# Kernel optimization log

Hardware: AMD Instinct MI355X
Metric: run time of the kernel (lower is better)

The kernel has to match this reference:

```python
import jax, jax.numpy as jnp
import numpy as np

N_NODES = 100000
N_EDGES = 600000
F_IN, HID, CLS = 128, 128, 16


def sage_conv(x, src, dst, W_l, b_l, W_r, n_nodes):
    # mean aggregation of neighbor features: message x[src] scattered to dst
    msg = x[src]                                              # [E, F]
    agg = jax.ops.segment_sum(msg, dst, num_segments=n_nodes)  # [N, F]
    deg = jax.ops.segment_sum(jnp.ones((src.shape[0],), x.dtype), dst, num_segments=n_nodes)
    agg = agg / jnp.maximum(deg, 1.0)[:, None]
    # PyG SAGEConv: lin_l(agg) (with bias) + lin_r(x_root) (no bias)
    return agg @ W_l + b_l + x @ W_r


def setup_inputs() -> dict:
    key = jax.random.key(0)
    ks = jax.random.split(key, 6)
    x = jax.random.normal(ks[0], (N_NODES, F_IN), jnp.float32)
    edge_index = jax.random.randint(ks[1], (2, N_EDGES), 0, N_NODES, dtype=jnp.int64)
    s1 = 1.0 / np.sqrt(F_IN)
    s2 = 1.0 / np.sqrt(HID)
    return {
        "x": x,
        "edge_index": edge_index,
        "W1_l": jax.random.normal(ks[2], (F_IN, HID), jnp.float32) * s1,
        "b1": jnp.zeros((HID,), jnp.float32),
        "W1_r": jax.random.normal(ks[3], (F_IN, HID), jnp.float32) * s1,
        "W2_l": jax.random.normal(ks[4], (HID, CLS), jnp.float32) * s2,
        "b2": jnp.zeros((CLS,), jnp.float32),
        "W2_r": jax.random.normal(ks[5], (HID, CLS), jnp.float32) * s2,
    }


def reference(x, edge_index, W1_l, b1, W1_r, W2_l, b2, W2_r):
    n = x.shape[0]
    src, dst = edge_index[0], edge_index[1]
    h = sage_conv(x, src, dst, W1_l, b1, W1_r, n)
    h = jax.nn.relu(h)
    # F.dropout(training=self.training): identity in eval mode
    out = sage_conv(h, src, dst, W2_l, b2, W2_r, n)
    return jax.nn.log_softmax(out, axis=1)
```

## Files before the change

kernel.cpp:

```cpp
#include <hip/hip_runtime.h>
#include <cstdint>

#define N_NODES 100000
#define N_PAD 100096
#define N_EDGES 600000
#define F 128
#define CLS 16
#define CAP 32

typedef short bf16x8 __attribute__((ext_vector_type(8)));
typedef float f32x4 __attribute__((ext_vector_type(4)));

__device__ inline float bf2f(unsigned int lo16) { return __uint_as_float(lo16 << 16); }
__device__ inline unsigned short f2b(float f) {
    unsigned int u = __float_as_uint(f);
    return (unsigned short)((u + 0x7fffu + ((u >> 16) & 1u)) >> 16);
}

__global__ __launch_bounds__(256) void prep_k(const int* __restrict__ src,
                                              const int* __restrict__ dst,
                                              int* __restrict__ deg,
                                              int* __restrict__ bucket,
                                              const float* __restrict__ x,
                                              unsigned short* __restrict__ xb,
                                              const float* __restrict__ W1l,
                                              const float* __restrict__ W1r,
                                              const float* __restrict__ W2l,
                                              const float* __restrict__ W2r,
                                              unsigned short* __restrict__ w1t,
                                              unsigned short* __restrict__ w2t) {
    int b = blockIdx.x;
    if (b < 2344) {
        int e = b * 256 + threadIdx.x;
        if (e < N_EDGES) {
            int d = dst[e];
            int slot = atomicAdd(&deg[d], 1);
            if (slot < CAP) bucket[d * CAP + slot] = src[e];
        }
    } else if (b < 14844) {
        int i = (b - 2344) * 256 + threadIdx.x;
        float4 v = ((const float4*)x)[i];
        ushort4 o;
        o.x = f2b(v.x); o.y = f2b(v.y); o.z = f2b(v.z); o.w = f2b(v.w);
        ((ushort4*)xb)[i] = o;
    } else if (b < 14972) {
        int idx = (b - 14844) * 256 + threadIdx.x;
        int n = idx >> 8, k = idx & 255;
        float v = (k < F) ? W1l[k * F + n] : W1r[(k - F) * F + n];
        int ct = n >> 4, m = n & 15;
        int half = k >> 7, ks = (k >> 5) & 3, quad = (k >> 3) & 3, j = k & 7;
        w1t[(ct * 8 + ks * 2 + half) * 512 + (quad * 16 + m) * 8 + j] = f2b(v);
    } else {
        int idx = (b - 14972) * 256 + threadIdx.x;
        if (idx < 32 * F) {
            int n = idx >> 7, k = idx & 127;
            float v = (n < CLS) ? W2l[k * CLS + n] : W2r[k * CLS + (n - CLS)];
            int tile = n >> 4, m = n & 15;
            int ks = (k >> 5) & 3, quad = (k >> 3) & 3, j = k & 7;
            w2t[(tile * 4 + ks) * 512 + (quad * 16 + m) * 8 + j] = f2b(v);
        }
    }
}

__global__ __launch_bounds__(256) void gemm_fused(const unsigned short* __restrict__ Xb,
                                                  const int* __restrict__ deg,
                                                  const int* __restrict__ bucket,
                                                  const unsigned short* __restrict__ Wt,
                                                  const float* __restrict__ bias,
                                                  const unsigned short* __restrict__ Wt2,
                                                  unsigned short* __restrict__ trLb,
                                                  float* __restrict__ trR) {
    __shared__ unsigned short sh[128 * 136];
    int tid = threadIdx.x;
    int row0 = blockIdx.x * 128;

    {
        int ns = tid >> 1, half = tid & 1;
        const int4* gsrc = (const int4*)(bucket + (size_t)(row0 + ns) * CAP + half * 16);
        int* drow = (int*)(sh + ns * 136);
        int4* ldst = (int4*)(drow + half * 16);
        ldst[0] = gsrc[0];
        ldst[1] = gsrc[1];
        ldst[2] = gsrc[2];
        ldst[3] = gsrc[3];
        if (half == 0) drow[32] = deg[row0 + ns];
    }

    int grp = tid >> 5, c4 = (tid & 31) * 4;
    int lrb = grp * 16;

#define ISSUE(P, DV, LR) do { \
    const int* brow_ = (const int*)(sh + (LR) * 136); \
    int node_ = row0 + (LR); \
    int draw_ = brow_[32]; \
    DV = (node_ < N_NODES) ? min(max(draw_, 0), CAP) : 0; \
    int4 b0_ = ((const int4*)brow_)[0]; \
    int4 b1_ = ((const int4*)brow_)[1]; \
    int4 b2_ = ((const int4*)brow_)[2]; \
    int n0_  = (DV > 0 ) ? min(max(b0_.x, 0), N_NODES - 1) : 0; \
    int n1_  = (DV > 1 ) ? min(max(b0_.y, 0), N_NODES - 1) : 0; \
    int n2_  = (DV > 2 ) ? min(max(b0_.z, 0), N_NODES - 1) : 0; \
    int n3_  = (DV > 3 ) ? min(max(b0_.w, 0), N_NODES - 1) : 0; \
    int n4_  = (DV > 4 ) ? min(max(b1_.x, 0), N_NODES - 1) : 0; \
    int n5_  = (DV > 5 ) ? min(max(b1_.y, 0), N_NODES - 1) : 0; \
    int n6_  = (DV > 6 ) ? min(max(b1_.z, 0), N_NODES - 1) : 0; \
    int n7_  = (DV > 7 ) ? min(max(b1_.w, 0), N_NODES - 1) : 0; \
    int n8_  = (DV > 8 ) ? min(max(b2_.x, 0), N_NODES - 1) : 0; \
    int n9_  = (DV > 9 ) ? min(max(b2_.y, 0), N_NODES - 1) : 0; \
    int n10_ = (DV > 10) ? min(max(b2_.z, 0), N_NODES - 1) : 0; \
    int n11_ = (DV > 11) ? min(max(b2_.w, 0), N_NODES - 1) : 0; \
    P##0  = *(const uint2*)(Xb + (size_t)n0_  * F + c4); \
    P##1  = *(const uint2*)(Xb + (size_t)n1_  * F + c4); \
    P##2  = *(const uint2*)(Xb + (size_t)n2_  * F + c4); \
    P##3  = *(const uint2*)(Xb + (size_t)n3_  * F + c4); \
    P##4  = *(const uint2*)(Xb + (size_t)n4_  * F + c4); \
    P##5  = *(const uint2*)(Xb + (size_t)n5_  * F + c4); \
    P##6  = *(const uint2*)(Xb + (size_t)n6_  * F + c4); \
    P##7  = *(const uint2*)(Xb + (size_t)n7_  * F + c4); \
    P##8  = *(const uint2*)(Xb + (size_t)n8_  * F + c4); \
    P##9  = *(const uint2*)(Xb + (size_t)n9_  * F + c4); \
    P##10 = *(const uint2*)(Xb + (size_t)n10_ * F + c4); \
    P##11 = *(const uint2*)(Xb + (size_t)n11_ * F + c4); \
} while (0)

#define ACC4(vv) { \
    acc_[0] += bf2f((vv).x & 0xffffu); acc_[1] += bf2f((vv).x >> 16); \
    acc_[2] += bf2f((vv).y & 0xffffu); acc_[3] += bf2f((vv).y >> 16); }

#define CONSUME(P, DV, LR) do { \
    float acc_[4] = {0.f, 0.f, 0.f, 0.f}; \
    if (DV > 0)  ACC4(P##0); \
    if (DV > 1)  ACC4(P##1); \
    if (DV > 2)  ACC4(P##2); \
    if (DV > 3)  ACC4(P##3); \
    if (DV > 4)  ACC4(P##4); \
    if (DV > 5)  ACC4(P##5); \
    if (DV > 6)  ACC4(P##6); \
    if (DV > 7)  ACC4(P##7); \
    if (DV > 8)  ACC4(P##8); \
    if (DV > 9)  ACC4(P##9); \
    if (DV > 10) ACC4(P##10); \
    if (DV > 11) ACC4(P##11); \
    if (DV > 12) { \
        const int* brow_ = (const int*)(sh + (LR) * 136); \
        for (int j0 = 12; j0 < DV; j0 += 4) { \
            int4 bb_ = *(const int4*)(brow_ + j0); \
            int rem_ = DV - j0; \
            int m0_ = (rem_ > 0) ? min(max(bb_.x, 0), N_NODES - 1) : 0; \
            int m1_ = (rem_ > 1) ? min(max(bb_.y, 0), N_NODES - 1) : 0; \
            int m2_ = (rem_ > 2) ? min(max(bb_.z, 0), N_NODES - 1) : 0; \
            int m3_ = (rem_ > 3) ? min(max(bb_.w, 0), N_NODES - 1) : 0; \
            uint2 w0_ = *(const uint2*)(Xb + (size_t)m0_ * F + c4); \
            uint2 w1_ = *(const uint2*)(Xb + (size_t)m1_ * F + c4); \
            uint2 w2_ = *(const uint2*)(Xb + (size_t)m2_ * F + c4); \
            uint2 w3_ = *(const uint2*)(Xb + (size_t)m3_ * F + c4); \
            if (rem_ > 0) ACC4(w0_); \
            if (rem_ > 1) ACC4(w1_); \
            if (rem_ > 2) ACC4(w2_); \
            if (rem_ > 3) ACC4(w3_); \
        } \
    } \
    float inv_ = 1.0f / fmaxf((float)DV, 1.0f); \
    uint2 o_; \
    o_.x = (unsigned int)f2b(acc_[0] * inv_) | ((unsigned int)f2b(acc_[1] * inv_) << 16); \
    o_.y = (unsigned int)f2b(acc_[2] * inv_) | ((unsigned int)f2b(acc_[3] * inv_) << 16); \
    *(uint2*)&sh[(LR) * 136 + c4] = o_; \
} while (0)

    {
        uint2 vA0, vA1, vA2, vA3, vA4, vA5, vA6, vA7, vA8, vA9, vA10, vA11;
        uint2 vB0, vB1, vB2, vB3, vB4, vB5, vB6, vB7, vB8, vB9, vB10, vB11;
        int dA, dB;
        ISSUE(vA, dA, lrb + 0);
        ISSUE(vB, dB, lrb + 1);
#pragma unroll 1
        for (int rr = 0; rr < 14; rr += 2) {
            CONSUME(vA, dA, lrb + rr);
            ISSUE(vA, dA, lrb + rr + 2);
            CONSUME(vB, dB, lrb + rr + 1);
            ISSUE(vB, dB, lrb + rr + 3);
        }
        CONSUME(vA, dA, lrb + 14);
        CONSUME(vB, dB, lrb + 15);
    }
#undef ISSUE
#undef ACC4
#undef CONSUME
    __syncthreads();

    int wave = tid >> 6, lane = tid & 63;
    int m = lane & 15, quad = lane >> 4;
    int koff = quad * 8;
    int wrow0 = row0 + wave * 32;

    const unsigned short* sa0 = sh + (wave * 32 + m) * 136 + koff;
    const unsigned short* sa1 = sa0 + 16 * 136;
    const unsigned short* px0 = Xb + (size_t)(wrow0 + m) * F + koff;
    const unsigned short* px1 = px0 + 16 * F;
    const unsigned short* pw = Wt + lane * 8;

    f32x4 acc0[8], acc1[8];
#pragma unroll
    for (int ct = 0; ct < 8; ct++) { acc0[ct] = (f32x4){0,0,0,0}; acc1[ct] = (f32x4){0,0,0,0}; }

#pragma unroll
    for (int ks = 0; ks < 4; ks++) {
        bf16x8 a0 = *(const bf16x8*)(const void*)(sa0 + ks * 32);
        bf16x8 a1 = *(const bf16x8*)(const void*)(sa1 + ks * 32);
        bf16x8 x0 = *(const bf16x8*)(const void*)(px0 + ks * 32);
        bf16x8 x1 = *(const bf16x8*)(const void*)(px1 + ks * 32);
#pragma unroll
        for (int ct = 0; ct < 8; ct++) {
            bf16x8 bl = *(const bf16x8*)(const void*)(pw + (ct * 8 + ks * 2 + 0) * 512);
            bf16x8 br = *(const bf16x8*)(const void*)(pw + (ct * 8 + ks * 2 + 1) * 512);
            acc0[ct] = __builtin_amdgcn_mfma_f32_16x16x32_bf16(a0, bl, acc0[ct], 0, 0, 0);
            acc1[ct] = __builtin_amdgcn_mfma_f32_16x16x32_bf16(a1, bl, acc1[ct], 0, 0, 0);
            acc0[ct] = __builtin_amdgcn_mfma_f32_16x16x32_bf16(x0, br, acc0[ct], 0, 0, 0);
            acc1[ct] = __builtin_amdgcn_mfma_f32_16x16x32_bf16(x1, br, acc1[ct], 0, 0, 0);
        }
    }
    __syncthreads();

    int lr0 = wave * 32 + quad * 4;
#pragma unroll
    for (int ct = 0; ct < 8; ct++) {
        int n = ct * 16 + m;
        float bv = bias[n];
#pragma unroll
        for (int r = 0; r < 4; r++) {
            sh[(lr0 + r) * 136 + n]      = f2b(fmaxf(acc0[ct][r] + bv, 0.f));
            sh[(lr0 + 16 + r) * 136 + n] = f2b(fmaxf(acc1[ct][r] + bv, 0.f));
        }
    }
    __syncthreads();

    const unsigned short* hl0 = sh + (wave * 32 + m) * 136 + koff;
    const unsigned short* hl1 = hl0 + 16 * 136;
    const unsigned short* pw2 = Wt2 + lane * 8;

    f32x4 al0 = (f32x4){0,0,0,0}, al1 = (f32x4){0,0,0,0};
    f32x4 ar0 = (f32x4){0,0,0,0}, ar1 = (f32x4){0,0,0,0};
#pragma unroll
    for (int ks = 0; ks < 4; ks++) {
        bf16x8 h0 = *(const bf16x8*)(const void*)(hl0 + ks * 32);
        bf16x8 h1 = *(const bf16x8*)(const void*)(hl1 + ks * 32);
        bf16x8 wl = *(const bf16x8*)(const void*)(pw2 + (0 * 4 + ks) * 512);
        bf16x8 wr = *(const bf16x8*)(const void*)(pw2 + (1 * 4 + ks) * 512);
        al0 = __builtin_amdgcn_mfma_f32_16x16x32_bf16(h0, wl, al0, 0, 0, 0);
        al1 = __builtin_amdgcn_mfma_f32_16x16x32_bf16(h1, wl, al1, 0, 0, 0);
        ar0 = __builtin_amdgcn_mfma_f32_16x16x32_bf16(h0, wr, ar0, 0, 0, 0);
        ar1 = __builtin_amdgcn_mfma_f32_16x16x32_bf16(h1, wr, ar1, 0, 0, 0);
    }
    int r0 = wrow0 + quad * 4;
#pragma unroll
    for (int r = 0; r < 4; r++) {
        trLb[(size_t)(r0 + r) * CLS + m]      = f2b(al0[r]);
        trLb[(size_t)(r0 + 16 + r) * CLS + m] = f2b(al1[r]);
        trR[(size_t)(r0 + r) * CLS + m]       = ar0[r];
        trR[(size_t)(r0 + 16 + r) * CLS + m]  = ar1[r];
    }
}

__global__ __launch_bounds__(256) void agg2sm_k(const unsigned short* __restrict__ trLb,
                                                const float* __restrict__ trR,
                                                const int* __restrict__ deg,
                                                const int* __restrict__ bucket,
                                                const float* __restrict__ b2,
                                                float* __restrict__ out) {
    int node = blockIdx.x * 4 + (threadIdx.x >> 6);
    int lane = threadIdx.x & 63;
    int r = lane >> 2;
    int cq = (lane & 3) * 4;
    const int* bk = bucket + node * CAP;

    int d_raw = deg[node];
    int d = min(d_raw, CAP);
    int nb = (r < d) ? min(max(bk[r], 0), N_NODES - 1) : 0;
    uint2 v = *(const uint2*)(trLb + (size_t)nb * CLS + cq);
    float4 selfR = *(const float4*)(trR + (size_t)node * CLS + cq);

    float4 acc = {0.f, 0.f, 0.f, 0.f};
    if (r < d) {
        acc.x += bf2f(v.x & 0xffffu); acc.y += bf2f(v.x >> 16);
        acc.z += bf2f(v.y & 0xffffu); acc.w += bf2f(v.y >> 16);
    }
    if (d > 16) {
        int idx = 16 + r;
        bool valid = idx < d;
        int m2 = valid ? min(max(bk[idx], 0), N_NODES - 1) : 0;
        uint2 w = *(const uint2*)(trLb + (size_t)m2 * CLS + cq);
        if (valid) {
            acc.x += bf2f(w.x & 0xffffu); acc.y += bf2f(w.x >> 16);
            acc.z += bf2f(w.y & 0xffffu); acc.w += bf2f(w.y >> 16);
        }
    }
#pragma unroll
    for (int off = 4; off <= 32; off <<= 1) {
        acc.x += __shfl_xor(acc.x, off);
        acc.y += __shfl_xor(acc.y, off);
        acc.z += __shfl_xor(acc.z, off);
        acc.w += __shfl_xor(acc.w, off);
    }
    float inv = 1.0f / fmaxf((float)d, 1.0f);
    float4 bb = *(const float4*)(b2 + cq);
    float vx = acc.x * inv + selfR.x + bb.x;
    float vy = acc.y * inv + selfR.y + bb.y;
    float vz = acc.z * inv + selfR.z + bb.z;
    float vw = acc.w * inv + selfR.w + bb.w;
    float mx = fmaxf(fmaxf(vx, vy), fmaxf(vz, vw));
    mx = fmaxf(mx, __shfl_xor(mx, 1));
    mx = fmaxf(mx, __shfl_xor(mx, 2));
    float sm = __expf(vx - mx) + __expf(vy - mx) + __expf(vz - mx) + __expf(vw - mx);
    sm += __shfl_xor(sm, 1);
    sm += __shfl_xor(sm, 2);
    float lg = __logf(sm);
    if (r == 0) {
        float4 o = {vx - mx - lg, vy - mx - lg, vz - mx - lg, vw - mx - lg};
        *(float4*)(out + (size_t)node * CLS + cq) = o;
    }
}


extern "C" void kernel_launch(void* const* d_in, const int* in_sizes, int n_in,
                              void* d_out, int out_size, void* d_ws, size_t ws_size,
                              hipStream_t stream) {
    const float* x   = (const float*)d_in[0];
    const int*   ei  = (const int*)d_in[1];
    const float* W1l = (const float*)d_in[2];
    const float* b1  = (const float*)d_in[3];
    const float* W1r = (const float*)d_in[4];
    const float* W2l = (const float*)d_in[5];
    const float* b2  = (const float*)d_in[6];
    const float* W2r = (const float*)d_in[7];
    float* out = (float*)d_out;

    const int* src = ei;
    const int* dst = ei + N_EDGES;

    char* ws = (char*)d_ws;
    size_t off = 0;
    auto alloc = [&](size_t bytes) { char* p = ws + off; off += (bytes + 127) / 128 * 128; return p; };
    int* deg    = (int*)alloc((size_t)N_NODES * 4);
    int* bucket = (int*)alloc((size_t)N_NODES * CAP * 4);
    unsigned short* xb   = (unsigned short*)alloc((size_t)N_PAD * F * 2);
    unsigned short* trLb = (unsigned short*)alloc((size_t)N_PAD * CLS * 2);
    float*          trR  = (float*)alloc((size_t)N_PAD * CLS * 4);
    unsigned short* w1t  = (unsigned short*)alloc((size_t)F * 256 * 2);
    unsigned short* w2t  = (unsigned short*)alloc((size_t)32 * F * 2);

    hipMemsetAsync(deg, 0, (size_t)N_NODES * 4, stream);
    prep_k<<<14988, 256, 0, stream>>>(src, dst, deg, bucket, x, xb,
                                      W1l, W1r, W2l, W2r, w1t, w2t);
    gemm_fused<<<N_PAD / 128, 256, 0, stream>>>(xb, deg, bucket, w1t, b1, w2t, trLb, trR);
    agg2sm_k<<<N_NODES / 4, 256, 0, stream>>>(trLb, trR, deg, bucket, b2, out);
}
```

Measured before the change: 218.6 us.

## Gather neighbor rows into LDS via global_load_lds instead of register prefetch

Replaces the register-based software-pipelined neighbor gather (two nodes in flight, 12 uint2 loads each) with direct global-to-LDS 16-byte loads into a per-wave scratch buffer, then sums from LDS. Each wave handles two nodes per step, waiting on vmcnt(0) before consuming, so there is no overlap between gather and accumulate across steps. It aims to issue wider loads and reduce register pressure, at the cost of extra LDS usage (which may lower occupancy) and a serialized load-wait per step.

```diff
diff --git a/kernel.cpp b/kernel.cpp
--- a/kernel.cpp
+++ b/kernel.cpp
@@ -7,6 +7,7 @@
 #define F 128
 #define CLS 16
 #define CAP 32
+#define SLOTS 12
 
 typedef short bf16x8 __attribute__((ext_vector_type(8)));
 typedef float f32x4 __attribute__((ext_vector_type(4)));
@@ -71,8 +72,10 @@
                                                   unsigned short* __restrict__ trLb,
                                                   float* __restrict__ trR) {
     __shared__ unsigned short sh[128 * 136];
+    __shared__ unsigned short scr[4][2 * SLOTS * 128];
     int tid = threadIdx.x;
     int row0 = blockIdx.x * 128;
+    int wave = tid >> 6, lane = tid & 63;
 
     {
         int ns = tid >> 1, half = tid & 1;
@@ -86,109 +89,66 @@
         if (half == 0) drow[32] = deg[row0 + ns];
     }
 
-    int grp = tid >> 5, c4 = (tid & 31) * 4;
-    int lrb = grp * 16;
-
-#define ISSUE(P, DV, LR) do { \
-    const int* brow_ = (const int*)(sh + (LR) * 136); \
-    int node_ = row0 + (LR); \
-    int draw_ = brow_[32]; \
-    DV = (node_ < N_NODES) ? min(max(draw_, 0), CAP) : 0; \
-    int4 b0_ = ((const int4*)brow_)[0]; \
-    int4 b1_ = ((const int4*)brow_)[1]; \
-    int4 b2_ = ((const int4*)brow_)[2]; \
-    int n0_  = (DV > 0 ) ? min(max(b0_.x, 0), N_NODES - 1) : 0; \
-    int n1_  = (DV > 1 ) ? min(max(b0_.y, 0), N_NODES - 1) : 0; \
-    int n2_  = (DV > 2 ) ? min(max(b0_.z, 0), N_NODES - 1) : 0; \
-    int n3_  = (DV > 3 ) ? min(max(b0_.w, 0), N_NODES - 1) : 0; \
-    int n4_  = (DV > 4 ) ? min(max(b1_.x, 0), N_NODES - 1) : 0; \
-    int n5_  = (DV > 5 ) ? min(max(b1_.y, 0), N_NODES - 1) : 0; \
-    int n6_  = (DV > 6 ) ? min(max(b1_.z, 0), N_NODES - 1) : 0; \
-    int n7_  = (DV > 7 ) ? min(max(b1_.w, 0), N_NODES - 1) : 0; \
-    int n8_  = (DV > 8 ) ? min(max(b2_.x, 0), N_NODES - 1) : 0; \
-    int n9_  = (DV > 9 ) ? min(max(b2_.y, 0), N_NODES - 1) : 0; \
-    int n10_ = (DV > 10) ? min(max(b2_.z, 0), N_NODES - 1) : 0; \
-    int n11_ = (DV > 11) ? min(max(b2_.w, 0), N_NODES - 1) : 0; \
-    P##0  = *(const uint2*)(Xb + (size_t)n0_  * F + c4); \
-    P##1  = *(const uint2*)(Xb + (size_t)n1_  * F + c4); \
-    P##2  = *(const uint2*)(Xb + (size_t)n2_  * F + c4); \
-    P##3  = *(const uint2*)(Xb + (size_t)n3_  * F + c4); \
-    P##4  = *(const uint2*)(Xb + (size_t)n4_  * F + c4); \
-    P##5  = *(const uint2*)(Xb + (size_t)n5_  * F + c4); \
-    P##6  = *(const uint2*)(Xb + (size_t)n6_  * F + c4); \
-    P##7  = *(const uint2*)(Xb + (size_t)n7_  * F + c4); \
-    P##8  = *(const uint2*)(Xb + (size_t)n8_  * F + c4); \
-    P##9  = *(const uint2*)(Xb + (size_t)n9_  * F + c4); \
-    P##10 = *(const uint2*)(Xb + (size_t)n10_ * F + c4); \
-    P##11 = *(const uint2*)(Xb + (size_t)n11_ * F + c4); \
-} while (0)
-
-#define ACC4(vv) { \
-    acc_[0] += bf2f((vv).x & 0xffffu); acc_[1] += bf2f((vv).x >> 16); \
-    acc_[2] += bf2f((vv).y & 0xffffu); acc_[3] += bf2f((vv).y >> 16); }
-
-#define CONSUME(P, DV, LR) do { \
-    float acc_[4] = {0.f, 0.f, 0.f, 0.f}; \
-    if (DV > 0)  ACC4(P##0); \
-    if (DV > 1)  ACC4(P##1); \
-    if (DV > 2)  ACC4(P##2); \
-    if (DV > 3)  ACC4(P##3); \
-    if (DV > 4)  ACC4(P##4); \
-    if (DV > 5)  ACC4(P##5); \
-    if (DV > 6)  ACC4(P##6); \
-    if (DV > 7)  ACC4(P##7); \
-    if (DV > 8)  ACC4(P##8); \
-    if (DV > 9)  ACC4(P##9); \
-    if (DV > 10) ACC4(P##10); \
-    if (DV > 11) ACC4(P##11); \
-    if (DV > 12) { \
-        const int* brow_ = (const int*)(sh + (LR) * 136); \
-        for (int j0 = 12; j0 < DV; j0 += 4) { \
-            int4 bb_ = *(const int4*)(brow_ + j0); \
-            int rem_ = DV - j0; \
-            int m0_ = (rem_ > 0) ? min(max(bb_.x, 0), N_NODES - 1) : 0; \
-            int m1_ = (rem_ > 1) ? min(max(bb_.y, 0), N_NODES - 1) : 0; \
-            int m2_ = (rem_ > 2) ? min(max(bb_.z, 0), N_NODES - 1) : 0; \
-            int m3_ = (rem_ > 3) ? min(max(bb_.w, 0), N_NODES - 1) : 0; \
-            uint2 w0_ = *(const uint2*)(Xb + (size_t)m0_ * F + c4); \
-            uint2 w1_ = *(const uint2*)(Xb + (size_t)m1_ * F + c4); \
-            uint2 w2_ = *(const uint2*)(Xb + (size_t)m2_ * F + c4); \
-            uint2 w3_ = *(const uint2*)(Xb + (size_t)m3_ * F + c4); \
-            if (rem_ > 0) ACC4(w0_); \
-            if (rem_ > 1) ACC4(w1_); \
-            if (rem_ > 2) ACC4(w2_); \
-            if (rem_ > 3) ACC4(w3_); \
-        } \
-    } \
-    float inv_ = 1.0f / fmaxf((float)DV, 1.0f); \
-    uint2 o_; \
-    o_.x = (unsigned int)f2b(acc_[0] * inv_) | ((unsigned int)f2b(acc_[1] * inv_) << 16); \
-    o_.y = (unsigned int)f2b(acc_[2] * inv_) | ((unsigned int)f2b(acc_[3] * inv_) << 16); \
-    *(uint2*)&sh[(LR) * 136 + c4] = o_; \
-} while (0)
-
     {
-        uint2 vA0, vA1, vA2, vA3, vA4, vA5, vA6, vA7, vA8, vA9, vA10, vA11;
-        uint2 vB0, vB1, vB2, vB3, vB4, vB5, vB6, vB7, vB8, vB9, vB10, vB11;
-        int dA, dB;
-        ISSUE(vA, dA, lrb + 0);
-        ISSUE(vB, dB, lrb + 1);
+        int l4 = lane >> 4;
+        int c16 = (lane & 15) * 8;
+        int nis = lane >> 5;
+        int c4 = (lane & 31) * 4;
+        unsigned short* myscr = &scr[wave][0];
+
 #pragma unroll 1
-        for (int rr = 0; rr < 14; rr += 2) {
-            CONSUME(vA, dA, lrb + rr);
-            ISSUE(vA, dA, lrb + rr + 2);
-            CONSUME(vB, dB, lrb + rr + 1);
-            ISSUE(vB, dB, lrb + rr + 3);
-        }
-        CONSUME(vA, dA, lrb + 14);
-        CONSUME(vB, dB, lrb + 15);
-    }
-#undef ISSUE
-#undef ACC4
-#undef CONSUME
+        for (int sc = 0; sc < 16; ++sc) {
+            int lrA = wave * 32 + sc * 2;
+            int lrB = lrA + 1;
+            const int* browA = (const int*)(sh + lrA * 136);
+            const int* browB = (const int*)(sh + lrB * 136);
+            int dAr = browA[32], dBr = browB[32];
+            int dA = (row0 + lrA < N_NODES) ? min(max(dAr, 0), CAP) : 0;
+            int dB = (row0 + lrB < N_NODES) ? min(max(dBr, 0), CAP) : 0;
+
+#pragma unroll
+            for (int i = 0; i < 6; ++i) {
+                const int* brow = (i < 3) ? browA : browB;
+                int dcl = (i < 3) ? dA : dB;
+                int slot = (i < 3 ? i * 4 : (i - 3) * 4) + l4;
+                int bs = brow[slot];
+                int nid = (slot < dcl) ? min(max(bs, 0), N_NODES - 1) : 0;
+                const unsigned short* gsrc = Xb + (size_t)nid * F + c16;
+                __builtin_amdgcn_global_load_lds(
+                    (const __attribute__((address_space(1))) unsigned int*)gsrc,
+                    (__attribute__((address_space(3))) unsigned int*)(myscr + (size_t)i * 512),
+                    16, 0, 0);
+            }
+            asm volatile("s_waitcnt vmcnt(0)" ::: "memory");
+            __builtin_amdgcn_sched_barrier(0);
+
+            int d_n = nis ? dB : dA;
+            const int* brow = nis ? browB : browA;
+            int lr = lrA + nis;
+            float a0 = 0.f, a1 = 0.f, a2 = 0.f, a3 = 0.f;
+#pragma unroll
+            for (int s = 0; s < SLOTS; ++s) {
+                uint2 v = *(const uint2*)&myscr[(nis * SLOTS + s) * 128 + c4];
+                if (d_n > s) {
+                    a0 += bf2f(v.x & 0xffffu); a1 += bf2f(v.x >> 16);
+                    a2 += bf2f(v.y & 0xffffu); a3 += bf2f(v.y >> 16);
+                }
+            }
+            for (int s = SLOTS; s < d_n; ++s) {
+                int nid = min(max(brow[s], 0), N_NODES - 1);
+                uint2 w = *(const uint2*)(Xb + (size_t)nid * F + c4);
+                a0 += bf2f(w.x & 0xffffu); a1 += bf2f(w.x >> 16);
+                a2 += bf2f(w.y & 0xffffu); a3 += bf2f(w.y >> 16);
+            }
+            float inv = 1.0f / fmaxf((float)d_n, 1.0f);
+            uint2 o;
+            o.x = (unsigned int)f2b(a0 * inv) | ((unsigned int)f2b(a1 * inv) << 16);
+            o.y = (unsigned int)f2b(a2 * inv) | ((unsigned int)f2b(a3 * inv) << 16);
+            *(uint2*)&sh[lr * 136 + c4] = o;
+        }
+    }
     __syncthreads();
 
-    int wave = tid >> 6, lane = tid & 63;
     int m = lane & 15, quad = lane >> 4;
     int koff = quad * 8;
     int wrow0 = row0 + wave * 32;
```

New measurement: 223.9 us. 2.4% more time.
